# Optimization experiments

Measured on AMD Instinct MI355X. Metric: run time of the kernel, lower is better.

## Reference

```python
import jax, jax.numpy as jnp
import numpy as np

B, K, U, D = 4096, 32, 16384, 256


def setup_inputs() -> dict:
    key = jax.random.key(0)
    k1, k2, k3 = jax.random.split(key, 3)
    neigh_idx = jax.random.randint(k1, (B, K), 0, U, dtype=jnp.int32)
    # emulate samp_neigh.union({node_id}): guarantee self index in each row
    neigh_idx = neigh_idx.at[:, 0].set(jnp.arange(B, dtype=jnp.int32))
    features_table = jax.random.normal(k2, (U, D), dtype=jnp.float32)
    noise_table = jax.random.normal(k3, (U, D), dtype=jnp.float32)
    return {"neigh_idx": neigh_idx, "features_table": features_table, "noise_table": noise_table}


def reference(neigh_idx, features_table, noise_table):
    # Dense binary mask [B, U]; duplicates collapse via .set (set semantics, as in torch mask[r,c]=1.0)
    rows = jnp.arange(neigh_idx.shape[0])[:, None]
    mask = jnp.zeros((neigh_idx.shape[0], features_table.shape[0]), features_table.dtype)
    mask = mask.at[rows, neigh_idx].set(1.0)
    # symmetric GCN normalization: mask / sqrt(rowsum) / sqrt(colsum)
    row_n = jnp.sqrt(mask.sum(axis=1, keepdims=True))  # >= 1 (self-loop present)
    col_n = jnp.sqrt(mask.sum(axis=0, keepdims=True))
    # In torch, unique_nodes_list only contains referenced nodes, so no zero columns.
    # Guard zero columns (mask entries there are 0, so result is unchanged vs torch).
    col_n = jnp.where(col_n > 0, col_n, 1.0)
    m = mask / row_n / col_n  # [B, U]
    to_feats = m @ features_table       # [B, D]
    to_noise_feats = m @ noise_table    # [B, D]
    return (to_feats, to_noise_feats)
```

## Files before the change

kernel.cpp:

```cpp
#include <hip/hip_runtime.h>


#define B_ 4096
#define K_ 32
#define U_ 16384
#define D_ 256
#define NPHASE 8
#define PHASE_SHIFT 11

__device__ __forceinline__ unsigned bf16_rne(float x) {
    const unsigned u = __float_as_uint(x);
    return (u + 0x7FFFu + ((u >> 16) & 1u)) >> 16;
}
__device__ __forceinline__ unsigned pack2(float lo, float hi) {
    return bf16_rne(lo) | (bf16_rne(hi) << 16);
}
__device__ __forceinline__ float blo(unsigned v) { return __uint_as_float(v << 16); }
__device__ __forceinline__ float bhi(unsigned v) { return __uint_as_float(v & 0xFFFF0000u); }

__global__ __launch_bounds__(256) void gcn_prep(const float4* __restrict__ feat,
                                                const float4* __restrict__ noise,
                                                uint4* __restrict__ packed,
                                                int* __restrict__ colcnt) {
    const int gid = blockIdx.x * 256 + threadIdx.x;
    if (gid < U_) colcnt[gid] = 0;

    const int half = U_ * D_ / 8;
    const bool isNoise = gid >= half;
    const int t = isNoise ? gid - half : gid;
    const int u = t >> 5;
    const int s = t & 31;

    const float4* src = isNoise ? noise : feat;
    const float4 a = src[u * (D_ / 4) + s * 2];
    const float4 b = src[u * (D_ / 4) + s * 2 + 1];

    uint4 o;
    o.x = pack2(a.x, a.y);
    o.y = pack2(a.z, a.w);
    o.z = pack2(b.x, b.y);
    o.w = pack2(b.z, b.w);
    packed[u * 64 + (isNoise ? 32 : 0) + s] = o;
}

__global__ __launch_bounds__(256) void gcn_colcount(const int* __restrict__ idx,
                                                    int* __restrict__ colcnt) {
    const int wave = (blockIdx.x * blockDim.x + threadIdx.x) >> 6;
    const int lane = threadIdx.x & 63;
    if (wave >= B_) return;

    const int kk = lane & 31;
    const int u = idx[wave * K_ + kk];

    bool dup = false;
    #pragma unroll
    for (int j = 0; j < K_; ++j) {
        const int uj = __shfl(u, j);
        if (j < kk && uj == u) dup = true;
    }
    if (lane < 32 && !dup) atomicAdd(&colcnt[u], 1);
}

__global__ __launch_bounds__(256) void gcn_gather(const int* __restrict__ idx,
                                                  const uint4* __restrict__ packed,
                                                  const int* __restrict__ colcnt,
                                                  float4* __restrict__ out) {
    const int row = blockIdx.x * 4 + (threadIdx.x >> 6);
    const int lane = threadIdx.x & 63;

    const int kk = lane & 31;
    const int u = idx[row * K_ + kk];

    bool dup = false;
    #pragma unroll
    for (int j = 0; j < K_; ++j) {
        const int uj = __shfl(u, j);
        if (j < kk && uj == u) dup = true;
    }
    const int rowcnt = __popcll(__ballot(!dup) & 0xFFFFFFFFull);

    float w = 0.0f;
    if (!dup) w = rsqrtf((float)(rowcnt * colcnt[u]));

    int   us[K_]; float wk[K_];
    #pragma unroll
    for (int k = 0; k < K_; ++k) {
        us[k] = __builtin_amdgcn_readlane(u, k);
        wk[k] = __uint_as_float(
            (unsigned)__builtin_amdgcn_readlane((int)__float_as_uint(w), k));
    }

    float a0 = 0.f, a1 = 0.f, a2 = 0.f, a3 = 0.f;
    float a4 = 0.f, a5 = 0.f, a6 = 0.f, a7 = 0.f;

    for (int p = 0; p < NPHASE; ++p) {
        #pragma unroll
        for (int k = 0; k < K_; ++k) {
            if ((us[k] >> PHASE_SHIFT) == p) {
                const uint4 v = packed[us[k] * 64 + lane];
                const float wkk = wk[k];
                a0 = fmaf(wkk, blo(v.x), a0);
                a1 = fmaf(wkk, bhi(v.x), a1);
                a2 = fmaf(wkk, blo(v.y), a2);
                a3 = fmaf(wkk, bhi(v.y), a3);
                a4 = fmaf(wkk, blo(v.z), a4);
                a5 = fmaf(wkk, bhi(v.z), a5);
                a6 = fmaf(wkk, blo(v.w), a6);
                a7 = fmaf(wkk, bhi(v.w), a7);
            }
        }
    }

    const int base = (lane < 32) ? (row * (D_ / 4) + lane * 2)
                                 : (B_ * (D_ / 4) + row * (D_ / 4) + (lane - 32) * 2);
    out[base]     = make_float4(a0, a1, a2, a3);
    out[base + 1] = make_float4(a4, a5, a6, a7);
}

extern "C" void kernel_launch(void* const* d_in, const int* in_sizes, int n_in,
                              void* d_out, int out_size, void* d_ws, size_t ws_size,
                              hipStream_t stream) {
    const int*    idx   = (const int*)d_in[0];
    const float4* feat  = (const float4*)d_in[1];
    const float4* noise = (const float4*)d_in[2];
    float4*       out   = (float4*)d_out;

    uint4* packed = (uint4*)d_ws;
    int*   colcnt = (int*)((char*)d_ws + 32u * 1024 * 1024);

    gcn_prep<<<(2 * U_ * D_ / 8) / 256, 256, 0, stream>>>(feat, noise, packed, colcnt);
    gcn_colcount<<<B_ / 4, 256, 0, stream>>>(idx, colcnt);
    gcn_gather<<<B_ / 4, 256, 0, stream>>>(idx, packed, colcnt, out);
}
```

Baseline: 40.65 us.

## Split prep into feat/noise kernels, fuse colcount, drop gather phase loop

The single prep kernel is split into separate feature and noise conversion kernels, and the column-count pass is folded into the noise kernel. Stores to the packed bf16 table become nontemporal. The gather kernel drops its 8-phase ordering loop and issues all 32 neighbor loads in one unrolled loop, which exposes more memory-level parallelism but gives up whatever cache locality the phase ordering provided. The column counts rely on the zeroing in the first kernel having completed before the second kernel's atomics, which stream ordering guarantees.

```diff
diff --git a/kernel.cpp b/kernel.cpp
--- a/kernel.cpp
+++ b/kernel.cpp
@@ -5,8 +5,9 @@
 #define K_ 32
 #define U_ 16384
 #define D_ 256
-#define NPHASE 8
-#define PHASE_SHIFT 11
+#define HALF_SLOTS (U_ * D_ / 8)
+
+typedef unsigned int uint4n __attribute__((ext_vector_type(4)));
 
 __device__ __forceinline__ unsigned bf16_rne(float x) {
     const unsigned u = __float_as_uint(x);
@@ -18,51 +19,53 @@
 __device__ __forceinline__ float blo(unsigned v) { return __uint_as_float(v << 16); }
 __device__ __forceinline__ float bhi(unsigned v) { return __uint_as_float(v & 0xFFFF0000u); }
 
-__global__ __launch_bounds__(256) void gcn_prep(const float4* __restrict__ feat,
-                                                const float4* __restrict__ noise,
-                                                uint4* __restrict__ packed,
-                                                int* __restrict__ colcnt) {
-    const int gid = blockIdx.x * 256 + threadIdx.x;
-    if (gid < U_) colcnt[gid] = 0;
-
-    const int half = U_ * D_ / 8;
-    const bool isNoise = gid >= half;
-    const int t = isNoise ? gid - half : gid;
+__device__ __forceinline__ void conv_slot(const float4* __restrict__ src,
+                                          uint4n* __restrict__ packed,
+                                          int t, int half_off) {
     const int u = t >> 5;
     const int s = t & 31;
-
-    const float4* src = isNoise ? noise : feat;
     const float4 a = src[u * (D_ / 4) + s * 2];
     const float4 b = src[u * (D_ / 4) + s * 2 + 1];
-
-    uint4 o;
+    uint4n o;
     o.x = pack2(a.x, a.y);
     o.y = pack2(a.z, a.w);
     o.z = pack2(b.x, b.y);
     o.w = pack2(b.z, b.w);
-    packed[u * 64 + (isNoise ? 32 : 0) + s] = o;
+    __builtin_nontemporal_store(o, &packed[u * 64 + half_off + s]);
 }
 
-__global__ __launch_bounds__(256) void gcn_colcount(const int* __restrict__ idx,
-                                                    int* __restrict__ colcnt) {
-    const int wave = (blockIdx.x * blockDim.x + threadIdx.x) >> 6;
-    const int lane = threadIdx.x & 63;
-    if (wave >= B_) return;
+__global__ __launch_bounds__(256) void gcn_prep_feat(const float4* __restrict__ feat,
+                                                     uint4n* __restrict__ packed,
+                                                     int* __restrict__ colcnt) {
+    const int gid = blockIdx.x * 256 + threadIdx.x;
+    if (gid < U_) colcnt[gid] = 0;
+    conv_slot(feat, packed, gid, 0);
+}
 
-    const int kk = lane & 31;
-    const int u = idx[wave * K_ + kk];
+__global__ __launch_bounds__(256) void gcn_prep_noise(const int* __restrict__ idx,
+                                                      const float4* __restrict__ noise,
+                                                      uint4n* __restrict__ packed,
+                                                      int* __restrict__ colcnt) {
+    const int gid = blockIdx.x * 256 + threadIdx.x;
+    conv_slot(noise, packed, gid, 32);
 
-    bool dup = false;
-    #pragma unroll
-    for (int j = 0; j < K_; ++j) {
-        const int uj = __shfl(u, j);
-        if (j < kk && uj == u) dup = true;
+    const int wg = gid >> 6;
+    if (wg < B_) {
+        const int lane = threadIdx.x & 63;
+        const int kk = lane & 31;
+        const int u = idx[wg * K_ + kk];
+        bool dup = false;
+        #pragma unroll
+        for (int j = 0; j < K_; ++j) {
+            const int uj = __shfl(u, j);
+            if (j < kk && uj == u) dup = true;
+        }
+        if (lane < 32 && !dup) atomicAdd(&colcnt[u], 1);
     }
-    if (lane < 32 && !dup) atomicAdd(&colcnt[u], 1);
 }
 
 __global__ __launch_bounds__(256) void gcn_gather(const int* __restrict__ idx,
-                                                  const uint4* __restrict__ packed,
+                                                  const uint4n* __restrict__ packed,
                                                   const int* __restrict__ colcnt,
                                                   float4* __restrict__ out) {
     const int row = blockIdx.x * 4 + (threadIdx.x >> 6);
@@ -82,7 +85,7 @@
     float w = 0.0f;
     if (!dup) w = rsqrtf((float)(rowcnt * colcnt[u]));
 
-    int   us[K_]; float wk[K_];
+    int us[K_]; float wk[K_];
     #pragma unroll
     for (int k = 0; k < K_; ++k) {
         us[k] = __builtin_amdgcn_readlane(u, k);
@@ -93,26 +96,23 @@
     float a0 = 0.f, a1 = 0.f, a2 = 0.f, a3 = 0.f;
     float a4 = 0.f, a5 = 0.f, a6 = 0.f, a7 = 0.f;
 
-    for (int p = 0; p < NPHASE; ++p) {
-        #pragma unroll
-        for (int k = 0; k < K_; ++k) {
-            if ((us[k] >> PHASE_SHIFT) == p) {
-                const uint4 v = packed[us[k] * 64 + lane];
-                const float wkk = wk[k];
-                a0 = fmaf(wkk, blo(v.x), a0);
-                a1 = fmaf(wkk, bhi(v.x), a1);
-                a2 = fmaf(wkk, blo(v.y), a2);
-                a3 = fmaf(wkk, bhi(v.y), a3);
-                a4 = fmaf(wkk, blo(v.z), a4);
-                a5 = fmaf(wkk, bhi(v.z), a5);
-                a6 = fmaf(wkk, blo(v.w), a6);
-                a7 = fmaf(wkk, bhi(v.w), a7);
-            }
-        }
+    #pragma unroll
+    for (int k = 0; k < K_; ++k) {
+        const uint4n v = packed[us[k] * 64 + lane];
+        const float wkk = wk[k];
+        a0 = fmaf(wkk, blo(v.x), a0);
+        a1 = fmaf(wkk, bhi(v.x), a1);
+        a2 = fmaf(wkk, blo(v.y), a2);
+        a3 = fmaf(wkk, bhi(v.y), a3);
+        a4 = fmaf(wkk, blo(v.z), a4);
+        a5 = fmaf(wkk, bhi(v.z), a5);
+        a6 = fmaf(wkk, blo(v.w), a6);
+        a7 = fmaf(wkk, bhi(v.w), a7);
     }
 
-    const int base = (lane < 32) ? (row * (D_ / 4) + lane * 2)
-                                 : (B_ * (D_ / 4) + row * (D_ / 4) + (lane - 32) * 2);
+    const int base = (lane < 32)
+        ? (row * (D_ / 4) + lane * 2)
+        : (B_ * (D_ / 4) + row * (D_ / 4) + (lane - 32) * 2);
     out[base]     = make_float4(a0, a1, a2, a3);
     out[base + 1] = make_float4(a4, a5, a6, a7);
 }
@@ -125,10 +125,10 @@
     const float4* noise = (const float4*)d_in[2];
     float4*       out   = (float4*)d_out;
 
-    uint4* packed = (uint4*)d_ws;
-    int*   colcnt = (int*)((char*)d_ws + 32u * 1024 * 1024);
+    uint4n* packed = (uint4n*)d_ws;
+    int*    colcnt = (int*)((char*)d_ws + 32u * 1024 * 1024);
 
-    gcn_prep<<<(2 * U_ * D_ / 8) / 256, 256, 0, stream>>>(feat, noise, packed, colcnt);
-    gcn_colcount<<<B_ / 4, 256, 0, stream>>>(idx, colcnt);
-    gcn_gather<<<B_ / 4, 256, 0, stream>>>(idx, packed, colcnt, out);
+    gcn_prep_feat <<<HALF_SLOTS / 256, 256, 0, stream>>>(feat, packed, colcnt);
+    gcn_prep_noise<<<HALF_SLOTS / 256, 256, 0, stream>>>(idx, noise, packed, colcnt);
+    gcn_gather    <<<B_ / 4,          256, 0, stream>>>(idx, packed, colcnt, out);
 }
```

Result: no change. 40.20 us (median of 2 runs) (-1.1%).
